# Performance work log

Measured on AMD Instinct MI355X. Metric: run time of the kernel, lower is better.

Reference implementation:

```python
import jax, jax.numpy as jnp
import numpy as np

B, N, G, K, V = 4, 512, 8, 64, 32000


def setup_inputs() -> dict:
    key = jax.random.key(0)
    k1, k2, k3 = jax.random.split(key, 3)
    phi = jax.random.normal(k1, (B, N, G, K), dtype=jnp.float32)
    # psi initialized uniform(-0.5, 0.5) as in torch.nn.init.uniform_
    psi = jax.random.uniform(k2, (V, K), dtype=jnp.float32, minval=-0.5, maxval=0.5)
    # perm[h, v] = index of h^{-1} acting on vocab word v (data-dependent permutation)
    perm = jax.random.randint(k3, (G, V), 0, V, dtype=jnp.int64)
    return {"phi": phi, "psi": psi, "perm": perm}


def reference(phi, psi, perm):
    # For each group element h: logits[b,n,v] += dot(phi[b,n,h,:], psi[perm[h,v],:])
    # Gather psi rows per group element: [G, V, K]
    psi_g = psi[perm]
    logits = jnp.einsum("bnhk,hvk->bnv", phi, psi_g)  # [B, N, V]
    return jax.nn.softmax(logits, axis=-1)
```

## Files before the change

kernel.cpp:

```cpp
#include <hip/hip_runtime.h>
#include <math.h>


#define M_ROWS 2048
#define V_DIM  32000
#define C_DIM  512
#define G_DIM  8
#define K_DIM  64
#define BM     128
#define BV     128
#define BK     32
#define NVBLK  (V_DIM / BV)
#define NMT    (M_ROWS / BM)
#define NKT    (C_DIM / BK)
#define LDS_ROW 40

typedef _Float16 f16x8 __attribute__((ext_vector_type(8)));
typedef _Float16 f16x4 __attribute__((ext_vector_type(4)));
typedef float    f32x4 __attribute__((ext_vector_type(4)));


__device__ __forceinline__ void gl_lds16(const void* g, void* l) {
  __builtin_amdgcn_global_load_lds(
      (const __attribute__((address_space(1))) unsigned int*)g,
      (__attribute__((address_space(3))) unsigned int*)l, 16, 0, 0);
}

__global__ __launch_bounds__(256) void gdecode_prep_phi(
    const float* __restrict__ phi, _Float16* __restrict__ aws)
{
  const int ga   = blockIdx.x * 256 + threadIdx.x;
  const int g    = ga & 511;
  const int half = (ga >> 9) & 1;
  const int tile = ga >> 10;
  const int kq = g >> 7, r = g & 127;
  const int m  = (tile >> 4) * BM + r;
  const int k  = (tile & 15) * BK + kq * 8;
  const float4 x0 = *(const float4*)(phi + (size_t)m * C_DIM + k);
  const float4 x1 = *(const float4*)(phi + (size_t)m * C_DIM + k + 4);
  const float xs[8] = {x0.x, x0.y, x0.z, x0.w, x1.x, x1.y, x1.z, x1.w};
  f16x8 o;
  #pragma unroll
  for (int j = 0; j < 8; ++j) {
    _Float16 hi = (_Float16)xs[j];
    o[j] = half ? (_Float16)(xs[j] - (float)hi) : hi;
  }
  *(f16x8*)(aws + (size_t)ga * 8) = o;
}

__global__ __launch_bounds__(256) void gdecode_prep_psi(
    const float* __restrict__ psi, const int* __restrict__ perm, const int pstride,
    _Float16* __restrict__ bws)
{
  const int gb   = blockIdx.x * 256 + threadIdx.x;
  const int g    = gb & 511;
  const int tile = gb >> 9;
  const int it = tile / 250;
  const int vb = tile - it * 250;
  const int kq = g >> 7, r = g & 127;
  const int h   = it >> 1;
  const int kin = (it & 1) * 32 + kq * 8;
  const int v   = vb * BV + r;
  const int pr  = perm[(size_t)(h * V_DIM + v) * pstride];
  const float4 x0 = *(const float4*)(psi + (size_t)pr * K_DIM + kin);
  const float4 x1 = *(const float4*)(psi + (size_t)pr * K_DIM + kin + 4);
  f16x8 o = {(_Float16)x0.x, (_Float16)x0.y, (_Float16)x0.z, (_Float16)x0.w,
             (_Float16)x1.x, (_Float16)x1.y, (_Float16)x1.z, (_Float16)x1.w};
  *(f16x8*)(bws + (size_t)gb * 8) = o;
}

__global__ __launch_bounds__(256, 4) void gdecode_gemm2(
    const _Float16* __restrict__ aws, const _Float16* __restrict__ bws,
    float* __restrict__ out, float* __restrict__ smax, float* __restrict__ ssum)
{
  __shared__ __align__(16) _Float16 lds[3 * 4096];
  _Float16* sAh = lds;
  _Float16* sAl = lds + 4096;
  _Float16* sB  = lds + 8192;

  const int t  = threadIdx.x;
  const int vb = blockIdx.x;
  const int mt = blockIdx.y;
  const int vbase = vb * BV;
  const int mbase = mt * BM;

  const int wid  = t >> 6;
  const int lane = t & 63;
  const int wm   = wid & 1;
  const int wv   = wid >> 1;
  const int lrow = lane & 15;
  const int quad = lane >> 4;

  const _Float16* gA = aws + (size_t)mt * NKT * 2 * 4096;
  const _Float16* gB = bws + (size_t)vb * 4096;

  f32x4 acc[4][4] = {};

  for (int it = 0; it < 16; ++it) {
    __syncthreads();
    const _Float16* ga = gA + (size_t)it * 2 * 4096;
    const _Float16* gb = gB + (size_t)it * NVBLK * 4096;
    gl_lds16(ga + (size_t)t * 8,          sAh + t * 8);
    gl_lds16(ga + 2048 + (size_t)t * 8,   sAh + 2048 + t * 8);
    gl_lds16(ga + 4096 + (size_t)t * 8,   sAl + t * 8);
    gl_lds16(ga + 6144 + (size_t)t * 8,   sAl + 2048 + t * 8);
    gl_lds16(gb + (size_t)t * 8,          sB + t * 8);
    gl_lds16(gb + 2048 + (size_t)t * 8,   sB + 2048 + t * 8);
    __syncthreads();

    f16x8 ah[4], al[4], bf[4];
    #pragma unroll
    for (int i = 0; i < 4; ++i) {
      const int ra = quad * 1024 + (wm * 64 + i * 16 + lrow) * 8;
      const int rb = quad * 1024 + (wv * 64 + i * 16 + lrow) * 8;
      ah[i] = *(const f16x8*)(sAh + ra);
      al[i] = *(const f16x8*)(sAl + ra);
      bf[i] = *(const f16x8*)(sB + rb);
    }
    #pragma unroll
    for (int i = 0; i < 4; ++i) {
      #pragma unroll
      for (int j = 0; j < 4; ++j) {
        acc[i][j] = __builtin_amdgcn_mfma_f32_16x16x32_f16(ah[i], bf[j], acc[i][j], 0, 0, 0);
        acc[i][j] = __builtin_amdgcn_mfma_f32_16x16x32_f16(al[i], bf[j], acc[i][j], 0, 0, 0);
      }
    }
  }

  __syncthreads();
  float* redmax = (float*)lds;
  float* redsum = redmax + 2 * BM;
  const int rowb = wm * 64;

  #pragma unroll
  for (int i = 0; i < 4; ++i) {
    #pragma unroll
    for (int r = 0; r < 4; ++r) {
      float v = fmaxf(fmaxf(acc[i][0][r], acc[i][1][r]),
                      fmaxf(acc[i][2][r], acc[i][3][r]));
      v = fmaxf(v, __shfl_xor(v, 1));
      v = fmaxf(v, __shfl_xor(v, 2));
      v = fmaxf(v, __shfl_xor(v, 4));
      v = fmaxf(v, __shfl_xor(v, 8));
      if (lrow == 0) redmax[(rowb + i * 16 + quad * 4 + r) * 2 + wv] = v;
    }
  }
  __syncthreads();
  float gmx[4][4];
  #pragma unroll
  for (int i = 0; i < 4; ++i) {
    #pragma unroll
    for (int r = 0; r < 4; ++r) {
      int row = rowb + i * 16 + quad * 4 + r;
      gmx[i][r] = fmaxf(redmax[row * 2], redmax[row * 2 + 1]);
    }
  }
  #pragma unroll
  for (int i = 0; i < 4; ++i) {
    #pragma unroll
    for (int r = 0; r < 4; ++r) {
      float s = __expf(acc[i][0][r] - gmx[i][r]) + __expf(acc[i][1][r] - gmx[i][r])
              + __expf(acc[i][2][r] - gmx[i][r]) + __expf(acc[i][3][r] - gmx[i][r]);
      s += __shfl_xor(s, 1);
      s += __shfl_xor(s, 2);
      s += __shfl_xor(s, 4);
      s += __shfl_xor(s, 8);
      if (lrow == 0) redsum[(rowb + i * 16 + quad * 4 + r) * 2 + wv] = s;
    }
  }
  __syncthreads();
  if (t < BM) {
    size_t o = (size_t)vb * M_ROWS + mbase + t;
    smax[o] = fmaxf(redmax[t * 2], redmax[t * 2 + 1]);
    ssum[o] = redsum[t * 2] + redsum[t * 2 + 1];
  }
  #pragma unroll
  for (int i = 0; i < 4; ++i) {
    #pragma unroll
    for (int j = 0; j < 4; ++j) {
      #pragma unroll
      for (int r = 0; r < 4; ++r) {
        int grow = mbase + rowb + i * 16 + quad * 4 + r;
        int gcol = vbase + wv * 64 + j * 16 + lrow;
        __builtin_nontemporal_store(acc[i][j][r], out + (size_t)grow * V_DIM + gcol);
      }
    }
  }
}

__global__ __launch_bounds__(256) void gdecode_combine(
    const float* __restrict__ smax, const float* __restrict__ ssum,
    float* __restrict__ rowM, float* __restrict__ rowI)
{
  const int m = blockIdx.x * 256 + threadIdx.x;
  float Mv = -3.4e38f;
  #pragma unroll 5
  for (int vb = 0; vb < NVBLK; ++vb) Mv = fmaxf(Mv, smax[(size_t)vb * M_ROWS + m]);
  float S = 0.f;
  #pragma unroll 5
  for (int vb = 0; vb < NVBLK; ++vb)
    S += ssum[(size_t)vb * M_ROWS + m] * __expf(smax[(size_t)vb * M_ROWS + m] - Mv);
  rowM[m] = Mv;
  rowI[m] = 1.f / S;
}

__global__ __launch_bounds__(256) void gdecode_norm(
    float* __restrict__ out, const float* __restrict__ rowM, const float* __restrict__ rowI)
{
  const int m = blockIdx.x >> 2;
  const int c = blockIdx.x & 3;
  const float Mv = rowM[m];
  const float Iv = rowI[m];
  f32x4* row = (f32x4*)(out + (size_t)m * V_DIM + c * 8000);
  for (int i = threadIdx.x; i < 2000; i += 256) {
    f32x4 x = __builtin_nontemporal_load(row + i);
    f32x4 y;
    y[0] = __expf(x[0] - Mv) * Iv;
    y[1] = __expf(x[1] - Mv) * Iv;
    y[2] = __expf(x[2] - Mv) * Iv;
    y[3] = __expf(x[3] - Mv) * Iv;
    __builtin_nontemporal_store(y, row + i);
  }
}


__global__ __launch_bounds__(256, 2) void gdecode_gemm_fb(
    const float* __restrict__ phi, const float* __restrict__ psi,
    const int* __restrict__ perm, const int pstride,
    float* __restrict__ out, float* __restrict__ smax, float* __restrict__ ssum)
{
  __shared__ __align__(16) _Float16 lds[3 * BM * LDS_ROW];
  _Float16* sAhi = lds;
  _Float16* sAlo = lds + BM * LDS_ROW;
  _Float16* sB   = lds + 2 * BM * LDS_ROW;

  const int t     = threadIdx.x;
  const int vbase = blockIdx.x * BV;
  const int mbase = blockIdx.y * BM;

  const int kg = t & 7;
  const int r0 = t >> 3;

  const int wid  = t >> 6;
  const int lane = t & 63;
  const int wm   = wid & 1;
  const int wv   = wid >> 1;
  const int lrow = lane & 15;
  const int quad = lane >> 4;

  f32x4 acc[4][4] = {};

  for (int it = 0; it < 16; ++it) {
    const int cb  = it * BK;
    const int h   = cb >> 6;
    const int kin = cb & 63;

    float4 av[4], bv[4];
    #pragma unroll
    for (int i = 0; i < 4; ++i) {
      int m = r0 + i * 32;
      av[i] = *(const float4*)(phi + (size_t)(mbase + m) * C_DIM + cb + kg * 4);
    }
    #pragma unroll
    for (int i = 0; i < 4; ++i) {
      int v  = r0 + i * 32;
      int pr = perm[(size_t)(h * V_DIM + vbase + v) * pstride];
      bv[i]  = *(const float4*)(psi + (size_t)pr * K_DIM + kin + kg * 4);
    }

    __syncthreads();

    #pragma unroll
    for (int i = 0; i < 4; ++i) {
      int m = r0 + i * 32;
      float4 x = av[i];
      _Float16 h0 = (_Float16)x.x, h1 = (_Float16)x.y,
               h2 = (_Float16)x.z, h3 = (_Float16)x.w;
      f16x4 hi = {h0, h1, h2, h3};
      f16x4 lo = {(_Float16)(x.x - (float)h0), (_Float16)(x.y - (float)h1),
                  (_Float16)(x.z - (float)h2), (_Float16)(x.w - (float)h3)};
      *(f16x4*)(sAhi + m * LDS_ROW + kg * 4) = hi;
      *(f16x4*)(sAlo + m * LDS_ROW + kg * 4) = lo;
    }
    #pragma unroll
    for (int i = 0; i < 4; ++i) {
      int v = r0 + i * 32;
      float4 x = bv[i];
      f16x4 w = {(_Float16)x.x, (_Float16)x.y, (_Float16)x.z, (_Float16)x.w};
      *(f16x4*)(sB + v * LDS_ROW + kg * 4) = w;
    }

    __syncthreads();

    f16x8 ah[4], al[4], bf[4];
    #pragma unroll
    for (int i = 0; i < 4; ++i) {
      ah[i] = *(const f16x8*)(sAhi + (wm * 64 + i * 16 + lrow) * LDS_ROW + quad * 8);
      al[i] = *(const f16x8*)(sAlo + (wm * 64 + i * 16 + lrow) * LDS_ROW + quad * 8);
      bf[i] = *(const f16x8*)(sB   + (wv * 64 + i * 16 + lrow) * LDS_ROW + quad * 8);
    }
    #pragma unroll
    for (int i = 0; i < 4; ++i) {
      #pragma unroll
      for (int j = 0; j < 4; ++j) {
        acc[i][j] = __builtin_amdgcn_mfma_f32_16x16x32_f16(ah[i], bf[j], acc[i][j], 0, 0, 0);
        acc[i][j] = __builtin_amdgcn_mfma_f32_16x16x32_f16(al[i], bf[j], acc[i][j], 0, 0, 0);
      }
    }
  }

  __syncthreads();
  float* redmax = (float*)lds;
  float* redsum = redmax + 2 * BM;
  const int rowb = wm * 64;

  #pragma unroll
  for (int i = 0; i < 4; ++i) {
    #pragma unroll
    for (int r = 0; r < 4; ++r) {
      float v = fmaxf(fmaxf(acc[i][0][r], acc[i][1][r]),
                      fmaxf(acc[i][2][r], acc[i][3][r]));
      v = fmaxf(v, __shfl_xor(v, 1));
      v = fmaxf(v, __shfl_xor(v, 2));
      v = fmaxf(v, __shfl_xor(v, 4));
      v = fmaxf(v, __shfl_xor(v, 8));
      if (lrow == 0) redmax[(rowb + i * 16 + quad * 4 + r) * 2 + wv] = v;
    }
  }
  __syncthreads();
  float gmx[4][4];
  #pragma unroll
  for (int i = 0; i < 4; ++i) {
    #pragma unroll
    for (int r = 0; r < 4; ++r) {
      int row = rowb + i * 16 + quad * 4 + r;
      gmx[i][r] = fmaxf(redmax[row * 2], redmax[row * 2 + 1]);
    }
  }
  #pragma unroll
  for (int i = 0; i < 4; ++i) {
    #pragma unroll
    for (int r = 0; r < 4; ++r) {
      float s = __expf(acc[i][0][r] - gmx[i][r]) + __expf(acc[i][1][r] - gmx[i][r])
              + __expf(acc[i][2][r] - gmx[i][r]) + __expf(acc[i][3][r] - gmx[i][r]);
      s += __shfl_xor(s, 1);
      s += __shfl_xor(s, 2);
      s += __shfl_xor(s, 4);
      s += __shfl_xor(s, 8);
      if (lrow == 0) redsum[(rowb + i * 16 + quad * 4 + r) * 2 + wv] = s;
    }
  }
  __syncthreads();
  if (smax != nullptr && t < BM) {
    int row = t;
    size_t o = (size_t)(mbase + row) * NVBLK + blockIdx.x;
    smax[o] = fmaxf(redmax[row * 2], redmax[row * 2 + 1]);
    ssum[o] = redsum[row * 2] + redsum[row * 2 + 1];
  }
  #pragma unroll
  for (int i = 0; i < 4; ++i) {
    #pragma unroll
    for (int j = 0; j < 4; ++j) {
      #pragma unroll
      for (int r = 0; r < 4; ++r) {
        int grow = mbase + rowb + i * 16 + quad * 4 + r;
        int gcol = vbase + wv * 64 + j * 16 + lrow;
        out[(size_t)grow * V_DIM + gcol] = acc[i][j][r];
      }
    }
  }
}

__global__ __launch_bounds__(256) void gdecode_softmax_ws(
    float* __restrict__ out, const float* __restrict__ smax, const float* __restrict__ ssum)
{
  __shared__ float sbuf[4];
  const int m = blockIdx.x;
  const int t = threadIdx.x;
  const float* rm = smax + (size_t)m * NVBLK;
  const float* rs = ssum + (size_t)m * NVBLK;

  float lm = -3.4e38f;
  for (int i = t; i < NVBLK; i += 256) lm = fmaxf(lm, rm[i]);
  for (int d = 1; d < 64; d <<= 1) lm = fmaxf(lm, __shfl_xor(lm, d));
  if ((t & 63) == 0) sbuf[t >> 6] = lm;
  __syncthreads();
  const float M = fmaxf(fmaxf(sbuf[0], sbuf[1]), fmaxf(sbuf[2], sbuf[3]));
  __syncthreads();

  float ls = 0.f;
  for (int i = t; i < NVBLK; i += 256) ls += rs[i] * __expf(rm[i] - M);
  for (int d = 1; d < 64; d <<= 1) ls += __shfl_xor(ls, d);
  if ((t & 63) == 0) sbuf[t >> 6] = ls;
  __syncthreads();
  const float inv = 1.f / (sbuf[0] + sbuf[1] + sbuf[2] + sbuf[3]);

  float4* row = (float4*)(out + (size_t)m * V_DIM);
  for (int i = t; i < V_DIM / 4; i += 256) {
    float4 x = row[i];
    x.x = __expf(x.x - M) * inv;
    x.y = __expf(x.y - M) * inv;
    x.z = __expf(x.z - M) * inv;
    x.w = __expf(x.w - M) * inv;
    row[i] = x;
  }
}

__global__ __launch_bounds__(256) void gdecode_softmax_nows(float* __restrict__ out)
{
  __shared__ float sbuf[4];
  const int m = blockIdx.x;
  const int t = threadIdx.x;
  float4* row = (float4*)(out + (size_t)m * V_DIM);

  float lm = -3.4e38f;
  for (int i = t; i < V_DIM / 4; i += 256) {
    float4 x = row[i];
    lm = fmaxf(lm, fmaxf(fmaxf(x.x, x.y), fmaxf(x.z, x.w)));
  }
  for (int d = 1; d < 64; d <<= 1) lm = fmaxf(lm, __shfl_xor(lm, d));
  if ((t & 63) == 0) sbuf[t >> 6] = lm;
  __syncthreads();
  const float M = fmaxf(fmaxf(sbuf[0], sbuf[1]), fmaxf(sbuf[2], sbuf[3]));
  __syncthreads();

  float ls = 0.f;
  for (int i = t; i < V_DIM / 4; i += 256) {
    float4 x = row[i];
    ls += __expf(x.x - M) + __expf(x.y - M) + __expf(x.z - M) + __expf(x.w - M);
  }
  for (int d = 1; d < 64; d <<= 1) ls += __shfl_xor(ls, d);
  if ((t & 63) == 0) sbuf[t >> 6] = ls;
  __syncthreads();
  const float inv = 1.f / (sbuf[0] + sbuf[1] + sbuf[2] + sbuf[3]);

  for (int i = t; i < V_DIM / 4; i += 256) {
    float4 x = row[i];
    x.x = __expf(x.x - M) * inv;
    x.y = __expf(x.y - M) * inv;
    x.z = __expf(x.z - M) * inv;
    x.w = __expf(x.w - M) * inv;
    row[i] = x;
  }
}


extern "C" void kernel_launch(void* const* d_in, const int* in_sizes, int n_in,
                              void* d_out, int out_size, void* d_ws, size_t ws_size,
                              hipStream_t stream)
{
  const float* phi  = (const float*)d_in[0];
  const float* psi  = (const float*)d_in[1];
  const int*   perm = (const int*)d_in[2];
  const int pstride = (in_sizes[2] == 2 * G_DIM * V_DIM) ? 2 : 1;

  float* out = (float*)d_out;

  const size_t AWS_B  = (size_t)NMT * NKT * 2 * 4096 * 2;
  const size_t BWS_B  = (size_t)NKT * NVBLK * 4096 * 2;
  const size_t STAT_B = (size_t)NVBLK * M_ROWS * 4;
  const size_t ROW_B  = (size_t)M_ROWS * 4;
  const size_t need_fast = AWS_B + BWS_B + 2 * STAT_B + 2 * ROW_B;

  if (d_ws != nullptr && ws_size >= need_fast) {
    char* wp = (char*)d_ws;
    _Float16* aws = (_Float16*)wp;                 wp += AWS_B;
    _Float16* bws = (_Float16*)wp;                 wp += BWS_B;
    float* smax   = (float*)wp;                    wp += STAT_B;
    float* ssum   = (float*)wp;                    wp += STAT_B;
    float* rowM   = (float*)wp;                    wp += ROW_B;
    float* rowI   = (float*)wp;

    gdecode_prep_phi<<<(NMT * NKT * 2 * 512) / 256, 256, 0, stream>>>(phi, aws);
    gdecode_prep_psi<<<(NKT * NVBLK * 512) / 256, 256, 0, stream>>>(psi, perm, pstride, bws);

    dim3 grid(NVBLK, NMT);
    gdecode_gemm2<<<grid, 256, 0, stream>>>(aws, bws, out, smax, ssum);

    gdecode_combine<<<M_ROWS / 256, 256, 0, stream>>>(smax, ssum, rowM, rowI);
    gdecode_norm<<<M_ROWS * 4, 256, 0, stream>>>(out, rowM, rowI);
    return;
  }

  const size_t need_old = (size_t)M_ROWS * NVBLK * 2 * sizeof(float);
  const bool hasws = (d_ws != nullptr) && (ws_size >= need_old);
  float* smax = hasws ? (float*)d_ws : nullptr;
  float* ssum = hasws ? smax + (size_t)M_ROWS * NVBLK : nullptr;

  dim3 grid(NVBLK, M_ROWS / BM);
  gdecode_gemm_fb<<<grid, 256, 0, stream>>>(phi, psi, perm, pstride, out, smax, ssum);

  if (hasws)
    gdecode_softmax_ws<<<M_ROWS, 256, 0, stream>>>(out, smax, ssum);
  else
    gdecode_softmax_nows<<<M_ROWS, 256, 0, stream>>>(out);
}
```

Baseline: 594.0 us.

## Double-buffer GEMM LDS staging, remap blocks per XCD, split combine reduction

The GEMM kernel now double-buffers its LDS tiles, prefetching the next K tile while MFMAs run on the current one, and drops one barrier per iteration. Blocks are remapped from a 1D grid so that each XCD handles a contiguous range of V blocks, which is meant to improve L2 reuse of the B tiles. The row-statistics combine, which used only 8 blocks to walk 250 partials serially, is split into two kernels (25 segments, then a final merge) to expose more parallelism. The norm kernel now uses a regular load instead of a nontemporal one. These add LDS usage, which may lower occupancy, plus an extra kernel launch and some idle blocks in the padded grid.

```diff
diff --git a/kernel.cpp b/kernel.cpp
--- a/kernel.cpp
+++ b/kernel.cpp
@@ -13,6 +13,9 @@
 #define NVBLK  (V_DIM / BV)
 #define NMT    (M_ROWS / BM)
 #define NKT    (C_DIM / BK)
+#define NSEG   25
+#define SEGV   (NVBLK / NSEG)
+#define LDSBUF 12288
 #define LDS_ROW 40
 
 typedef _Float16 f16x8 __attribute__((ext_vector_type(8)));
@@ -73,17 +76,19 @@
     const _Float16* __restrict__ aws, const _Float16* __restrict__ bws,
     float* __restrict__ out, float* __restrict__ smax, float* __restrict__ ssum)
 {
-  __shared__ __align__(16) _Float16 lds[3 * 4096];
-  _Float16* sAh = lds;
-  _Float16* sAl = lds + 4096;
-  _Float16* sB  = lds + 8192;
-
-  const int t  = threadIdx.x;
-  const int vb = blockIdx.x;
-  const int mt = blockIdx.y;
+  __shared__ __align__(16) _Float16 lds[2 * LDSBUF];
+
+  const int b   = blockIdx.x;
+  const int xcd = b & 7;
+  const int i   = b >> 3;
+  const int mt  = i >> 5;
+  const int vb  = xcd * 32 + (i & 31);
+  if (vb >= NVBLK) return;
+
   const int vbase = vb * BV;
   const int mbase = mt * BM;
 
+  const int t    = threadIdx.x;
   const int wid  = t >> 6;
   const int lane = t & 63;
   const int wm   = wid & 1;
@@ -94,78 +99,88 @@
   const _Float16* gA = aws + (size_t)mt * NKT * 2 * 4096;
   const _Float16* gB = bws + (size_t)vb * 4096;
 
-  f32x4 acc[4][4] = {};
-
-  for (int it = 0; it < 16; ++it) {
-    __syncthreads();
+  auto STAGE = [&](int it, _Float16* dst) {
     const _Float16* ga = gA + (size_t)it * 2 * 4096;
     const _Float16* gb = gB + (size_t)it * NVBLK * 4096;
-    gl_lds16(ga + (size_t)t * 8,          sAh + t * 8);
-    gl_lds16(ga + 2048 + (size_t)t * 8,   sAh + 2048 + t * 8);
-    gl_lds16(ga + 4096 + (size_t)t * 8,   sAl + t * 8);
-    gl_lds16(ga + 6144 + (size_t)t * 8,   sAl + 2048 + t * 8);
-    gl_lds16(gb + (size_t)t * 8,          sB + t * 8);
-    gl_lds16(gb + 2048 + (size_t)t * 8,   sB + 2048 + t * 8);
-    __syncthreads();
+    gl_lds16(ga + (size_t)t * 8,          dst + t * 8);
+    gl_lds16(ga + 2048 + (size_t)t * 8,   dst + 2048 + t * 8);
+    gl_lds16(ga + 4096 + (size_t)t * 8,   dst + 4096 + t * 8);
+    gl_lds16(ga + 6144 + (size_t)t * 8,   dst + 6144 + t * 8);
+    gl_lds16(gb + (size_t)t * 8,          dst + 8192 + t * 8);
+    gl_lds16(gb + 2048 + (size_t)t * 8,   dst + 8192 + 2048 + t * 8);
+  };
+
+  f32x4 acc[4][4] = {};
+
+  STAGE(0, lds);
+  __syncthreads();
+
+  for (int it = 0; it < 16; ++it) {
+    _Float16* cur = lds + (it & 1) * LDSBUF;
+    if (it < 15) STAGE(it + 1, lds + ((it & 1) ^ 1) * LDSBUF);
+
+    const _Float16* sAh = cur;
+    const _Float16* sAl = cur + 4096;
+    const _Float16* sB  = cur + 8192;
 
     f16x8 ah[4], al[4], bf[4];
     #pragma unroll
-    for (int i = 0; i < 4; ++i) {
-      const int ra = quad * 1024 + (wm * 64 + i * 16 + lrow) * 8;
-      const int rb = quad * 1024 + (wv * 64 + i * 16 + lrow) * 8;
-      ah[i] = *(const f16x8*)(sAh + ra);
-      al[i] = *(const f16x8*)(sAl + ra);
-      bf[i] = *(const f16x8*)(sB + rb);
-    }
-    #pragma unroll
-    for (int i = 0; i < 4; ++i) {
+    for (int k = 0; k < 4; ++k) {
+      const int ra = quad * 1024 + (wm * 64 + k * 16 + lrow) * 8;
+      const int rb = quad * 1024 + (wv * 64 + k * 16 + lrow) * 8;
+      ah[k] = *(const f16x8*)(sAh + ra);
+      al[k] = *(const f16x8*)(sAl + ra);
+      bf[k] = *(const f16x8*)(sB + rb);
+    }
+    #pragma unroll
+    for (int k = 0; k < 4; ++k) {
       #pragma unroll
       for (int j = 0; j < 4; ++j) {
-        acc[i][j] = __builtin_amdgcn_mfma_f32_16x16x32_f16(ah[i], bf[j], acc[i][j], 0, 0, 0);
-        acc[i][j] = __builtin_amdgcn_mfma_f32_16x16x32_f16(al[i], bf[j], acc[i][j], 0, 0, 0);
+        acc[k][j] = __builtin_amdgcn_mfma_f32_16x16x32_f16(ah[k], bf[j], acc[k][j], 0, 0, 0);
+        acc[k][j] = __builtin_amdgcn_mfma_f32_16x16x32_f16(al[k], bf[j], acc[k][j], 0, 0, 0);
       }
     }
-  }
-
-  __syncthreads();
+    __syncthreads();
+  }
+
   float* redmax = (float*)lds;
   float* redsum = redmax + 2 * BM;
   const int rowb = wm * 64;
 
   #pragma unroll
-  for (int i = 0; i < 4; ++i) {
+  for (int k = 0; k < 4; ++k) {
     #pragma unroll
     for (int r = 0; r < 4; ++r) {
-      float v = fmaxf(fmaxf(acc[i][0][r], acc[i][1][r]),
-                      fmaxf(acc[i][2][r], acc[i][3][r]));
+      float v = fmaxf(fmaxf(acc[k][0][r], acc[k][1][r]),
+                      fmaxf(acc[k][2][r], acc[k][3][r]));
       v = fmaxf(v, __shfl_xor(v, 1));
       v = fmaxf(v, __shfl_xor(v, 2));
       v = fmaxf(v, __shfl_xor(v, 4));
       v = fmaxf(v, __shfl_xor(v, 8));
-      if (lrow == 0) redmax[(rowb + i * 16 + quad * 4 + r) * 2 + wv] = v;
+      if (lrow == 0) redmax[(rowb + k * 16 + quad * 4 + r) * 2 + wv] = v;
     }
   }
   __syncthreads();
   float gmx[4][4];
   #pragma unroll
-  for (int i = 0; i < 4; ++i) {
+  for (int k = 0; k < 4; ++k) {
     #pragma unroll
     for (int r = 0; r < 4; ++r) {
-      int row = rowb + i * 16 + quad * 4 + r;
-      gmx[i][r] = fmaxf(redmax[row * 2], redmax[row * 2 + 1]);
-    }
-  }
-  #pragma unroll
-  for (int i = 0; i < 4; ++i) {
+      int row = rowb + k * 16 + quad * 4 + r;
+      gmx[k][r] = fmaxf(redmax[row * 2], redmax[row * 2 + 1]);
+    }
+  }
+  #pragma unroll
+  for (int k = 0; k < 4; ++k) {
     #pragma unroll
     for (int r = 0; r < 4; ++r) {
-      float s = __expf(acc[i][0][r] - gmx[i][r]) + __expf(acc[i][1][r] - gmx[i][r])
-              + __expf(acc[i][2][r] - gmx[i][r]) + __expf(acc[i][3][r] - gmx[i][r]);
+      float s = __expf(acc[k][0][r] - gmx[k][r]) + __expf(acc[k][1][r] - gmx[k][r])
+              + __expf(acc[k][2][r] - gmx[k][r]) + __expf(acc[k][3][r] - gmx[k][r]);
       s += __shfl_xor(s, 1);
       s += __shfl_xor(s, 2);
       s += __shfl_xor(s, 4);
       s += __shfl_xor(s, 8);
-      if (lrow == 0) redsum[(rowb + i * 16 + quad * 4 + r) * 2 + wv] = s;
+      if (lrow == 0) redsum[(rowb + k * 16 + quad * 4 + r) * 2 + wv] = s;
     }
   }
   __syncthreads();
@@ -175,31 +190,51 @@
     ssum[o] = redsum[t * 2] + redsum[t * 2 + 1];
   }
   #pragma unroll
-  for (int i = 0; i < 4; ++i) {
+  for (int k = 0; k < 4; ++k) {
     #pragma unroll
     for (int j = 0; j < 4; ++j) {
       #pragma unroll
       for (int r = 0; r < 4; ++r) {
-        int grow = mbase + rowb + i * 16 + quad * 4 + r;
+        int grow = mbase + rowb + k * 16 + quad * 4 + r;
         int gcol = vbase + wv * 64 + j * 16 + lrow;
-        __builtin_nontemporal_store(acc[i][j][r], out + (size_t)grow * V_DIM + gcol);
+        __builtin_nontemporal_store(acc[k][j][r], out + (size_t)grow * V_DIM + gcol);
       }
     }
   }
 }
 
-__global__ __launch_bounds__(256) void gdecode_combine(
+__global__ __launch_bounds__(256) void gdecode_combine1(
     const float* __restrict__ smax, const float* __restrict__ ssum,
+    float* __restrict__ pmax, float* __restrict__ psum)
+{
+  const int seg = blockIdx.x % NSEG;
+  const int m   = (blockIdx.x / NSEG) * 256 + threadIdx.x;
+  float Mv = -3.4e38f;
+  #pragma unroll
+  for (int j = 0; j < SEGV; ++j)
+    Mv = fmaxf(Mv, smax[(size_t)(seg * SEGV + j) * M_ROWS + m]);
+  float S = 0.f;
+  #pragma unroll
+  for (int j = 0; j < SEGV; ++j) {
+    const size_t o = (size_t)(seg * SEGV + j) * M_ROWS + m;
+    S += ssum[o] * __expf(smax[o] - Mv);
+  }
+  pmax[(size_t)seg * M_ROWS + m] = Mv;
+  psum[(size_t)seg * M_ROWS + m] = S;
+}
+
+__global__ __launch_bounds__(256) void gdecode_combine2(
+    const float* __restrict__ pmax, const float* __restrict__ psum,
     float* __restrict__ rowM, float* __restrict__ rowI)
 {
   const int m = blockIdx.x * 256 + threadIdx.x;
   float Mv = -3.4e38f;
-  #pragma unroll 5
-  for (int vb = 0; vb < NVBLK; ++vb) Mv = fmaxf(Mv, smax[(size_t)vb * M_ROWS + m]);
+  #pragma unroll
+  for (int s = 0; s < NSEG; ++s) Mv = fmaxf(Mv, pmax[(size_t)s * M_ROWS + m]);
   float S = 0.f;
-  #pragma unroll 5
-  for (int vb = 0; vb < NVBLK; ++vb)
-    S += ssum[(size_t)vb * M_ROWS + m] * __expf(smax[(size_t)vb * M_ROWS + m] - Mv);
+  #pragma unroll
+  for (int s = 0; s < NSEG; ++s)
+    S += psum[(size_t)s * M_ROWS + m] * __expf(pmax[(size_t)s * M_ROWS + m] - Mv);
   rowM[m] = Mv;
   rowI[m] = 1.f / S;
 }
@@ -213,7 +248,7 @@
   const float Iv = rowI[m];
   f32x4* row = (f32x4*)(out + (size_t)m * V_DIM + c * 8000);
   for (int i = threadIdx.x; i < 2000; i += 256) {
-    f32x4 x = __builtin_nontemporal_load(row + i);
+    f32x4 x = row[i];
     f32x4 y;
     y[0] = __expf(x[0] - Mv) * Iv;
     y[1] = __expf(x[1] - Mv) * Iv;
@@ -459,8 +494,9 @@
   const size_t AWS_B  = (size_t)NMT * NKT * 2 * 4096 * 2;
   const size_t BWS_B  = (size_t)NKT * NVBLK * 4096 * 2;
   const size_t STAT_B = (size_t)NVBLK * M_ROWS * 4;
+  const size_t PART_B = (size_t)NSEG * M_ROWS * 4;
   const size_t ROW_B  = (size_t)M_ROWS * 4;
-  const size_t need_fast = AWS_B + BWS_B + 2 * STAT_B + 2 * ROW_B;
+  const size_t need_fast = AWS_B + BWS_B + 2 * STAT_B + 2 * PART_B + 2 * ROW_B;
 
   if (d_ws != nullptr && ws_size >= need_fast) {
     char* wp = (char*)d_ws;
@@ -468,16 +504,18 @@
     _Float16* bws = (_Float16*)wp;                 wp += BWS_B;
     float* smax   = (float*)wp;                    wp += STAT_B;
     float* ssum   = (float*)wp;                    wp += STAT_B;
+    float* pmax   = (float*)wp;                    wp += PART_B;
+    float* psum   = (float*)wp;                    wp += PART_B;
     float* rowM   = (float*)wp;                    wp += ROW_B;
     float* rowI   = (float*)wp;
 
     gdecode_prep_phi<<<(NMT * NKT * 2 * 512) / 256, 256, 0, stream>>>(phi, aws);
     gdecode_prep_psi<<<(NKT * NVBLK * 512) / 256, 256, 0, stream>>>(psi, perm, pstride, bws);
 
-    dim3 grid(NVBLK, NMT);
-    gdecode_gemm2<<<grid, 256, 0, stream>>>(aws, bws, out, smax, ssum);
-
-    gdecode_combine<<<M_ROWS / 256, 256, 0, stream>>>(smax, ssum, rowM, rowI);
+    gdecode_gemm2<<<4096, 256, 0, stream>>>(aws, bws, out, smax, ssum);
+
+    gdecode_combine1<<<NSEG * (M_ROWS / 256), 256, 0, stream>>>(smax, ssum, pmax, psum);
+    gdecode_combine2<<<M_ROWS / 256, 256, 0, stream>>>(pmax, psum, rowM, rowI);
     gdecode_norm<<<M_ROWS * 4, 256, 0, stream>>>(out, rowM, rowI);
     return;
   }
```

New measurement: 542.8 us. 1.09x faster.
